# Performance work log

Hardware: AMD Instinct MI355X
Metric: run time of the kernel (lower is better)

## Reference

```python
import jax, jax.numpy as jnp
import numpy as np

BATCH, NEURONS, N_FEAT, IN_DIM, OUT_DIM = 256, 1024, 1024, 256, 128


def setup_inputs() -> dict:
    key = jax.random.key(0)
    kx, kg, kv, kw = jax.random.split(key, 4)
    x = jax.random.normal(kx, (BATCH, N_FEAT, IN_DIM), dtype=jnp.float32)
    G = jax.random.normal(kg, (NEURONS, N_FEAT), dtype=jnp.float32)
    # Original initializes v, w to zeros; use randn so outputs/grads are non-trivial.
    v = jax.random.normal(kv, (NEURONS, IN_DIM, OUT_DIM), dtype=jnp.float32)
    w = jax.random.normal(kw, (NEURONS, IN_DIM, OUT_DIM), dtype=jnp.float32)
    return {"x": x, "G": G, "v": v, "w": w}


def reference(x, G, v, w):
    # Original math: out[i,m] = sum_{j,k,l} G[j,k] * x[i,k,l] * (v - w)[j,l,m]
    # Reordered contraction: first G @ x (sum over feature axis k),
    # avoiding the quadratic (batch, neurons, n, in_dim) intermediate.
    Gx = jnp.einsum('jk,ikl->ijl', G, x)          # (batch, neurons, in_dim)
    return jnp.einsum('ijl,jlm->im', Gx, v - w)    # (batch, out_dim)
```

## Files before the change

kernel.cpp:

```cpp
#include <hip/hip_runtime.h>
#include <hip/hip_bf16.h>


typedef __attribute__((ext_vector_type(8))) short bf16x8;
typedef __attribute__((ext_vector_type(4))) float f32x4;

#define AS1C(p) ((const __attribute__((address_space(1))) void*)(p))
#define AS3(p)  ((__attribute__((address_space(3))) void*)(p))

__device__ __forceinline__ unsigned short f2bf(float f) {
    unsigned u = __float_as_uint(f);
    unsigned r = u + 0x7fffu + ((u >> 16) & 1u);
    return (unsigned short)(r >> 16);
}

__global__ void prep_G(const float* __restrict__ G, unsigned short* __restrict__ Gt) {
    __shared__ float tile[32][33];
    int k0 = blockIdx.x * 32, j0 = blockIdx.y * 32;
    int tx = threadIdx.x, ty = threadIdx.y;
    #pragma unroll
    for (int r = 0; r < 32; r += 8)
        tile[ty + r][tx] = G[(size_t)(j0 + ty + r) * 1024 + k0 + tx];
    __syncthreads();
    #pragma unroll
    for (int r = 0; r < 32; r += 8)
        Gt[(size_t)(k0 + ty + r) * 1024 + j0 + tx] = f2bf(tile[tx][ty + r]);
}

__global__ void prep_D(const float* __restrict__ v, const float* __restrict__ w,
                       unsigned short* __restrict__ Dt) {
    __shared__ unsigned short tile[32][132];
    int j0 = blockIdx.x * 32;
    int l  = blockIdx.y;
    int t  = threadIdx.x;
    #pragma unroll
    for (int it = 0; it < 16; ++it) {
        int idx = it * 256 + t;
        int j = idx >> 7, m = idx & 127;
        size_t g = (size_t)(j0 + j) * 32768 + (size_t)l * 128 + m;
        tile[j][m] = f2bf(v[g] - w[g]);
    }
    __syncthreads();
    int m = t >> 1, half = t & 1;
    unsigned short vals[16];
    #pragma unroll
    for (int q = 0; q < 16; ++q) vals[q] = tile[half * 16 + q][m];
    size_t dst = ((size_t)m * 256 + l) * 1024 + j0 + half * 16;
    *(uint4*)(Dt + dst)     = *(uint4*)(vals);
    *(uint4*)(Dt + dst + 8) = *(uint4*)(vals + 8);
}

__global__ __launch_bounds__(256) void gemm1(const unsigned short* __restrict__ Gt,
                                             const unsigned short* __restrict__ Dt,
                                             unsigned short* __restrict__ Tt) {
    __shared__ __align__(16) unsigned short As[128 * 32];
    __shared__ __align__(16) unsigned short Bs[128 * 32];
    int tid = threadIdx.x, wv = tid >> 6, lane = tid & 63;
    int k0 = blockIdx.x * 128, n0 = blockIdx.y * 128;
    int ldrow = lane >> 2, ldcol = (lane & 3) * 8;
    int wr = (wv >> 1) * 64, wc = (wv & 1) * 64;
    int quad = lane >> 4, l15 = lane & 15;

    f32x4 acc[4][4] = {};

    for (int j0 = 0; j0 < 1024; j0 += 32) {
        #pragma unroll
        for (int i = 0; i < 2; ++i) {
            int r = wv * 32 + i * 16;
            __builtin_amdgcn_global_load_lds(
                AS1C(Gt + (size_t)(k0 + r + ldrow) * 1024 + j0 + ldcol),
                AS3(As + r * 32), 16, 0, 0);
            __builtin_amdgcn_global_load_lds(
                AS1C(Dt + (size_t)(n0 + r + ldrow) * 1024 + j0 + ldcol),
                AS3(Bs + r * 32), 16, 0, 0);
        }
        __syncthreads();
        bf16x8 a[4], b[4];
        #pragma unroll
        for (int rt = 0; rt < 4; ++rt)
            a[rt] = *(const bf16x8*)(As + (wr + rt * 16 + l15) * 32 + quad * 8);
        #pragma unroll
        for (int ct = 0; ct < 4; ++ct)
            b[ct] = *(const bf16x8*)(Bs + (wc + ct * 16 + l15) * 32 + quad * 8);
        #pragma unroll
        for (int rt = 0; rt < 4; ++rt)
            #pragma unroll
            for (int ct = 0; ct < 4; ++ct)
                acc[rt][ct] = __builtin_amdgcn_mfma_f32_16x16x32_bf16(a[rt], b[ct], acc[rt][ct], 0, 0, 0);
        __syncthreads();
    }
    #pragma unroll
    for (int rt = 0; rt < 4; ++rt)
        #pragma unroll
        for (int ct = 0; ct < 4; ++ct) {
            int col = wc + ct * 16 + l15;
            int np  = n0 + col;
            int mm  = np >> 8, ll = np & 255;
            #pragma unroll
            for (int r = 0; r < 4; ++r) {
                int k = k0 + wr + rt * 16 + quad * 4 + r;
                Tt[(size_t)mm * 262144 + (size_t)k * 256 + ll] = f2bf(acc[rt][ct][r]);
            }
        }
}

__global__ __launch_bounds__(256) void gemm2(const float* __restrict__ x,
                                             const unsigned short* __restrict__ Tt,
                                             float* __restrict__ out) {
    __shared__ __align__(16) unsigned short Xs[64 * 32];
    __shared__ __align__(16) unsigned short Ts[128 * 32];
    int tid = threadIdx.x, wv = tid >> 6, lane = tid & 63;
    int i0 = blockIdx.x * 64;
    size_t kl0 = (size_t)blockIdx.y * 2048;
    int ldrow = lane >> 2, ldcol = (lane & 3) * 8;
    int wr = (wv >> 1) * 32, wc = (wv & 1) * 64;
    int quad = lane >> 4, l15 = lane & 15;

    f32x4 acc[2][4] = {};

    for (int it = 0; it < 64; ++it) {
        size_t kk = kl0 + it * 32;
        #pragma unroll
        for (int i = 0; i < 2; ++i) {
            int r = wv * 32 + i * 16;
            __builtin_amdgcn_global_load_lds(
                AS1C(Tt + (size_t)(r + ldrow) * 262144 + kk + ldcol),
                AS3(Ts + r * 32), 16, 0, 0);
        }
        #pragma unroll
        for (int i = 0; i < 2; ++i) {
            int f = tid + i * 256;
            int r = f >> 3, c = (f & 7) * 4;
            float4 xv = *(const float4*)(x + (size_t)(i0 + r) * 262144 + kk + c);
            unsigned short h[4] = {f2bf(xv.x), f2bf(xv.y), f2bf(xv.z), f2bf(xv.w)};
            *(uint2*)(Xs + r * 32 + c) = *(uint2*)h;
        }
        __syncthreads();
        bf16x8 a[2], b[4];
        #pragma unroll
        for (int rt = 0; rt < 2; ++rt)
            a[rt] = *(const bf16x8*)(Xs + (wr + rt * 16 + l15) * 32 + quad * 8);
        #pragma unroll
        for (int ct = 0; ct < 4; ++ct)
            b[ct] = *(const bf16x8*)(Ts + (wc + ct * 16 + l15) * 32 + quad * 8);
        #pragma unroll
        for (int rt = 0; rt < 2; ++rt)
            #pragma unroll
            for (int ct = 0; ct < 4; ++ct)
                acc[rt][ct] = __builtin_amdgcn_mfma_f32_16x16x32_bf16(a[rt], b[ct], acc[rt][ct], 0, 0, 0);
        __syncthreads();
    }
    #pragma unroll
    for (int rt = 0; rt < 2; ++rt)
        #pragma unroll
        for (int ct = 0; ct < 4; ++ct)
            #pragma unroll
            for (int r = 0; r < 4; ++r) {
                int i  = i0 + wr + rt * 16 + quad * 4 + r;
                int mo = wc + ct * 16 + l15;
                atomicAdd(&out[(size_t)i * 128 + mo], acc[rt][ct][r]);
            }
}

extern "C" void kernel_launch(void* const* d_in, const int* in_sizes, int n_in,
                              void* d_out, int out_size, void* d_ws, size_t ws_size,
                              hipStream_t stream) {
    const float* x = (const float*)d_in[0];
    const float* G = (const float*)d_in[1];
    const float* v = (const float*)d_in[2];
    const float* w = (const float*)d_in[3];
    float* out = (float*)d_out;

    char* ws = (char*)d_ws;
    unsigned short* Dt = (unsigned short*)(ws);
    unsigned short* Tt = (unsigned short*)(ws + 67108864);
    unsigned short* Gt = (unsigned short*)(ws + 134217728);

    hipMemsetAsync(d_out, 0, (size_t)256 * 128 * sizeof(float), stream);
    prep_G<<<dim3(32, 32), dim3(32, 8), 0, stream>>>(G, Gt);
    prep_D<<<dim3(32, 256), 256, 0, stream>>>(v, w, Dt);
    gemm1<<<dim3(8, 256), 256, 0, stream>>>(Gt, Dt, Tt);
    gemm2<<<dim3(4, 128), 256, 0, stream>>>(x, Tt, out);
}
```

Before: 686.4 us.

## Pipeline both GEMMs with multi-buffered LDS, larger tiles, and LDS-staged epilogue

gemm1 moves to 256x256 tiles with 512 threads. It uses a triple-buffered global_load_lds pipeline with explicit vmcnt waits and setprio around the MFMAs. Its output is staged through swizzled LDS so Tt is written with coalesced 16-byte stores. gemm2 gets a quad-buffered T pipeline, register-prefetched x loads with double-buffered X tiles, remapped block indices for L2 locality, and twice as many k-splits. The aim is to overlap memory latency with MFMA work and cut barrier stalls, at the cost of 128KB of LDS per gemm1 block, which limits occupancy, and more atomics in gemm2.

After: 659.2 us. 1.04x faster.

```diff
diff --git a/kernel.cpp b/kernel.cpp
--- a/kernel.cpp
+++ b/kernel.cpp
@@ -7,6 +7,7 @@
 
 #define AS1C(p) ((const __attribute__((address_space(1))) void*)(p))
 #define AS3(p)  ((__attribute__((address_space(3))) void*)(p))
+#define FENCE() asm volatile("" ::: "memory")
 
 __device__ __forceinline__ unsigned short f2bf(float f) {
     unsigned u = __float_as_uint(f);
@@ -50,92 +51,155 @@
     *(uint4*)(Dt + dst + 8) = *(uint4*)(vals + 8);
 }
 
-__global__ __launch_bounds__(256) void gemm1(const unsigned short* __restrict__ Gt,
-                                             const unsigned short* __restrict__ Dt,
-                                             unsigned short* __restrict__ Tt) {
-    __shared__ __align__(16) unsigned short As[128 * 32];
-    __shared__ __align__(16) unsigned short Bs[128 * 32];
+__global__ __launch_bounds__(512, 2) void gemm1(const unsigned short* __restrict__ Gt,
+                                                const unsigned short* __restrict__ Dt,
+                                                unsigned short* __restrict__ Tt) {
+    __shared__ __align__(16) unsigned short sm[65536];
     int tid = threadIdx.x, wv = tid >> 6, lane = tid & 63;
-    int k0 = blockIdx.x * 128, n0 = blockIdx.y * 128;
+    int n   = blockIdx.x;
+    int by  = ((n >> 5) << 3) + (n & 7);
+    int bx  = (n >> 3) & 3;
+    int k0 = bx * 256, n0 = by * 256;
+    int quad = lane >> 4, l15 = lane & 15;
+    int wr = (wv >> 2) * 128, wc = (wv & 3) * 64;
     int ldrow = lane >> 2, ldcol = (lane & 3) * 8;
-    int wr = (wv >> 1) * 64, wc = (wv & 1) * 64;
-    int quad = lane >> 4, l15 = lane & 15;
-
-    f32x4 acc[4][4] = {};
-
-    for (int j0 = 0; j0 < 1024; j0 += 32) {
-        #pragma unroll
-        for (int i = 0; i < 2; ++i) {
-            int r = wv * 32 + i * 16;
+    const unsigned short* gA = Gt + (size_t)k0 * 1024;
+    const unsigned short* gB = Dt + (size_t)n0 * 1024;
+
+    f32x4 acc[8][4] = {};
+
+    auto stage = [&](int slot, int jt) {
+        int j0 = jt * 32;
+        unsigned short* As = sm + slot * 16384;
+        unsigned short* Bs = As + 8192;
+        #pragma unroll
+        for (int i = 0; i < 2; ++i) {
+            int r = (wv * 2 + i) * 16;
             __builtin_amdgcn_global_load_lds(
-                AS1C(Gt + (size_t)(k0 + r + ldrow) * 1024 + j0 + ldcol),
-                AS3(As + r * 32), 16, 0, 0);
+                AS1C(gA + (size_t)(r + ldrow) * 1024 + j0 + ldcol), AS3(As + r * 32), 16, 0, 0);
             __builtin_amdgcn_global_load_lds(
-                AS1C(Dt + (size_t)(n0 + r + ldrow) * 1024 + j0 + ldcol),
-                AS3(Bs + r * 32), 16, 0, 0);
-        }
-        __syncthreads();
-        bf16x8 a[4], b[4];
-        #pragma unroll
-        for (int rt = 0; rt < 4; ++rt)
+                AS1C(gB + (size_t)(r + ldrow) * 1024 + j0 + ldcol), AS3(Bs + r * 32), 16, 0, 0);
+        }
+    };
+
+    stage(0, 0);
+    stage(1, 1);
+    int sR = 0;
+    for (int kt = 0; kt < 32; ++kt) {
+        if (kt + 1 < 32) asm volatile("s_waitcnt vmcnt(4)" ::: "memory");
+        else             asm volatile("s_waitcnt vmcnt(0)" ::: "memory");
+        __builtin_amdgcn_s_barrier();
+        FENCE();
+        if (kt + 2 < 32) {
+            int sW = sR + 2; if (sW >= 3) sW -= 3;
+            stage(sW, kt + 2);
+        }
+        const unsigned short* As = sm + sR * 16384;
+        const unsigned short* Bs = As + 8192;
+        bf16x8 a[8], b[4];
+        #pragma unroll
+        for (int rt = 0; rt < 8; ++rt)
             a[rt] = *(const bf16x8*)(As + (wr + rt * 16 + l15) * 32 + quad * 8);
         #pragma unroll
         for (int ct = 0; ct < 4; ++ct)
             b[ct] = *(const bf16x8*)(Bs + (wc + ct * 16 + l15) * 32 + quad * 8);
-        #pragma unroll
-        for (int rt = 0; rt < 4; ++rt)
+        __builtin_amdgcn_s_setprio(1);
+        #pragma unroll
+        for (int rt = 0; rt < 8; ++rt)
             #pragma unroll
             for (int ct = 0; ct < 4; ++ct)
                 acc[rt][ct] = __builtin_amdgcn_mfma_f32_16x16x32_bf16(a[rt], b[ct], acc[rt][ct], 0, 0, 0);
-        __syncthreads();
-    }
-    #pragma unroll
-    for (int rt = 0; rt < 4; ++rt)
-        #pragma unroll
-        for (int ct = 0; ct < 4; ++ct) {
-            int col = wc + ct * 16 + l15;
-            int np  = n0 + col;
-            int mm  = np >> 8, ll = np & 255;
+        __builtin_amdgcn_s_setprio(0);
+        sR = sR + 1; if (sR >= 3) sR = 0;
+    }
+
+    FENCE();
+    __builtin_amdgcn_s_barrier();
+    FENCE();
+    #pragma unroll
+    for (int rt = 0; rt < 8; ++rt)
+        #pragma unroll
+        for (int ct = 0; ct < 4; ++ct)
             #pragma unroll
             for (int r = 0; r < 4; ++r) {
-                int k = k0 + wr + rt * 16 + quad * 4 + r;
-                Tt[(size_t)mm * 262144 + (size_t)k * 256 + ll] = f2bf(acc[rt][ct][r]);
+                int row = wr + rt * 16 + quad * 4 + r;
+                int col = wc + ct * 16 + l15;
+                int byt = row * 512 + ((col * 2) ^ (((row >> 2) & 3) << 5));
+                *(unsigned short*)((char*)sm + byt) = f2bf(acc[rt][ct][r]);
             }
-        }
-}
-
-__global__ __launch_bounds__(256) void gemm2(const float* __restrict__ x,
-                                             const unsigned short* __restrict__ Tt,
-                                             float* __restrict__ out) {
-    __shared__ __align__(16) unsigned short Xs[64 * 32];
-    __shared__ __align__(16) unsigned short Ts[128 * 32];
+    asm volatile("s_waitcnt lgkmcnt(0)" ::: "memory");
+    __builtin_amdgcn_s_barrier();
+    FENCE();
+    int mm = n0 >> 8;
+    size_t base = (size_t)mm * 262144 + (size_t)k0 * 256;
+    #pragma unroll
+    for (int u = 0; u < 16; ++u) {
+        int c = u * 512 + tid;
+        int row = c >> 5, col16 = c & 31;
+        int byt = row * 512 + ((col16 * 16) ^ (((row >> 2) & 3) << 5));
+        *(uint4*)(Tt + base + (size_t)c * 8) = *(const uint4*)((const char*)sm + byt);
+    }
+}
+
+__global__ __launch_bounds__(256, 4) void gemm2(const float* __restrict__ x,
+                                                const unsigned short* __restrict__ Tt,
+                                                float* __restrict__ out) {
+    __shared__ __align__(16) unsigned short sm[4 * 4096 + 2 * 2048];
     int tid = threadIdx.x, wv = tid >> 6, lane = tid & 63;
-    int i0 = blockIdx.x * 64;
-    size_t kl0 = (size_t)blockIdx.y * 2048;
+    int n   = blockIdx.x;
+    int by  = ((n >> 5) << 3) + (n & 7);
+    int bx  = (n >> 3) & 3;
+    int i0 = bx * 64;
+    size_t kl0 = (size_t)by * 1024;
     int ldrow = lane >> 2, ldcol = (lane & 3) * 8;
     int wr = (wv >> 1) * 32, wc = (wv & 1) * 64;
     int quad = lane >> 4, l15 = lane & 15;
 
     f32x4 acc[2][4] = {};
-
-    for (int it = 0; it < 64; ++it) {
-        size_t kk = kl0 + it * 32;
-        #pragma unroll
-        for (int i = 0; i < 2; ++i) {
-            int r = wv * 32 + i * 16;
+    float4 xv[2];
+
+    auto stageT = [&](int slot, int t) {
+        size_t kk = kl0 + (size_t)t * 32;
+        unsigned short* Ts = sm + slot * 4096;
+        #pragma unroll
+        for (int i = 0; i < 2; ++i) {
+            int r = (wv * 2 + i) * 16;
             __builtin_amdgcn_global_load_lds(
-                AS1C(Tt + (size_t)(r + ldrow) * 262144 + kk + ldcol),
-                AS3(Ts + r * 32), 16, 0, 0);
-        }
+                AS1C(Tt + (size_t)(r + ldrow) * 262144 + kk + ldcol), AS3(Ts + r * 32), 16, 0, 0);
+        }
+    };
+    auto loadX = [&](int t) {
+        size_t kk = kl0 + (size_t)t * 32;
         #pragma unroll
         for (int i = 0; i < 2; ++i) {
             int f = tid + i * 256;
             int r = f >> 3, c = (f & 7) * 4;
-            float4 xv = *(const float4*)(x + (size_t)(i0 + r) * 262144 + kk + c);
-            unsigned short h[4] = {f2bf(xv.x), f2bf(xv.y), f2bf(xv.z), f2bf(xv.w)};
-            *(uint2*)(Xs + r * 32 + c) = *(uint2*)h;
-        }
-        __syncthreads();
+            xv[i] = *(const float4*)(x + (size_t)(i0 + r) * 262144 + kk + c);
+        }
+    };
+
+    loadX(0);
+    stageT(0, 0);
+    stageT(1, 1);
+
+    for (int kt = 0; kt < 32; ++kt) {
+        if (kt + 1 < 32) asm volatile("s_waitcnt vmcnt(2)" ::: "memory");
+        else             asm volatile("s_waitcnt vmcnt(0)" ::: "memory");
+        unsigned short* Xw = sm + 16384 + (kt & 1) * 2048;
+        #pragma unroll
+        for (int i = 0; i < 2; ++i) {
+            int f = tid + i * 256;
+            int r = f >> 3, c = (f & 7) * 4;
+            unsigned short h[4] = {f2bf(xv[i].x), f2bf(xv[i].y), f2bf(xv[i].z), f2bf(xv[i].w)};
+            *(uint2*)(Xw + r * 32 + c) = *(uint2*)h;
+        }
+        asm volatile("s_waitcnt lgkmcnt(0)" ::: "memory");
+        __builtin_amdgcn_s_barrier();
+        FENCE();
+        if (kt + 1 < 32) loadX(kt + 1);
+        if (kt + 2 < 32) stageT((kt + 2) & 3, kt + 2);
+        const unsigned short* Xs = sm + 16384 + (kt & 1) * 2048;
+        const unsigned short* Ts = sm + (kt & 3) * 4096;
         bf16x8 a[2], b[4];
         #pragma unroll
         for (int rt = 0; rt < 2; ++rt)
@@ -148,7 +212,6 @@
             #pragma unroll
             for (int ct = 0; ct < 4; ++ct)
                 acc[rt][ct] = __builtin_amdgcn_mfma_f32_16x16x32_bf16(a[rt], b[ct], acc[rt][ct], 0, 0, 0);
-        __syncthreads();
     }
     #pragma unroll
     for (int rt = 0; rt < 2; ++rt)
@@ -179,6 +242,6 @@
     hipMemsetAsync(d_out, 0, (size_t)256 * 128 * sizeof(float), stream);
     prep_G<<<dim3(32, 32), dim3(32, 8), 0, stream>>>(G, Gt);
     prep_D<<<dim3(32, 256), 256, 0, stream>>>(v, w, Dt);
-    gemm1<<<dim3(8, 256), 256, 0, stream>>>(Gt, Dt, Tt);
-    gemm2<<<dim3(4, 128), 256, 0, stream>>>(x, Tt, out);
-}
+    gemm1<<<512, 512, 0, stream>>>(Gt, Dt, Tt);
+    gemm2<<<1024, 256, 0, stream>>>(x, Tt, out);
+}
```
